# Kernel tuning notes

Hardware: AMD Instinct MI355X
Metric: run time of the kernel (lower is better)

The kernel has to match this reference:

```python
import jax, jax.numpy as jnp
import numpy as np
import math

N, E, H, NB, NL, NG, NELEM = 50000, 800000, 64, 8, 2, 64, 100
CUTOFF = 5.0


def _lin(k, fin, fout):
    kw, kb = jax.random.split(k)
    bound = 1.0 / math.sqrt(fin)
    w = jax.random.uniform(kw, (fin, fout), jnp.float32, -bound, bound)
    b = jax.random.uniform(kb, (fout,), jnp.float32, -bound, bound)
    return w, b


def setup_inputs() -> dict:
    key = jax.random.key(0)
    ks = jax.random.split(key, 12)
    z = jax.random.randint(ks[0], (N,), 0, NELEM)
    pos = jax.random.normal(ks[1], (N, 3), jnp.float32)
    edge_index = jax.random.randint(ks[2], (2, E), 0, N)
    batch = jnp.sort(jax.random.randint(ks[3], (N,), 0, NG))
    embed = jax.random.normal(ks[4], (NELEM, H), jnp.float32)
    # stacked per-interaction MLP params, leading dim = NL
    msg_w1, msg_b1, msg_w2, msg_b2 = [], [], [], []
    upd_w1, upd_b1, upd_w2, upd_b2 = [], [], [], []
    for l in range(NL):
        kl = jax.random.fold_in(ks[5], l)
        k1, k2, k3, k4 = jax.random.split(kl, 4)
        w, b = _lin(k1, 2 * H + NB, H); msg_w1.append(w); msg_b1.append(b)
        w, b = _lin(k2, H, H); msg_w2.append(w); msg_b2.append(b)
        w, b = _lin(k3, 2 * H, H); upd_w1.append(w); upd_b1.append(b)
        w, b = _lin(k4, H, H); upd_w2.append(w); upd_b2.append(b)
    eh_w1, eh_b1 = _lin(ks[6], H, H)
    eh_w2, eh_b2 = _lin(ks[7], H, 1)
    return {
        "z": z, "pos": pos, "edge_index": edge_index, "batch": batch,
        "embed": embed,
        "msg_w1": jnp.stack(msg_w1), "msg_b1": jnp.stack(msg_b1),
        "msg_w2": jnp.stack(msg_w2), "msg_b2": jnp.stack(msg_b2),
        "upd_w1": jnp.stack(upd_w1), "upd_b1": jnp.stack(upd_b1),
        "upd_w2": jnp.stack(upd_w2), "upd_b2": jnp.stack(upd_b2),
        "eh_w1": eh_w1, "eh_b1": eh_b1, "eh_w2": eh_w2, "eh_b2": eh_b2,
    }


def _mace_energy(pos, embed, msg_w1, msg_b1, msg_w2, msg_b2,
                 upd_w1, upd_b1, upd_w2, upd_b2,
                 eh_w1, eh_b1, eh_w2, eh_b2,
                 z, edge_index, batch):
    row, col = edge_index[0], edge_index[1]
    edge_vec = pos[row] - pos[col]                      # (E,3)
    d = jnp.linalg.norm(edge_vec, axis=-1)              # (E,)
    env = jnp.where(d < CUTOFF,
                    jnp.cos(d * (math.pi / (2 * CUTOFF))) ** 2,
                    0.0)
    freqs = jnp.arange(1, NB + 1, dtype=pos.dtype) * (math.pi / CUTOFF)
    d_safe = jnp.where(d > 0, d, 1.0)[:, None]
    edge_attr = jnp.sin(freqs * d[:, None]) / d_safe * env[:, None]  # (E,NB)

    x = embed[z]                                        # (N,H)
    for l in range(NL):
        # PyG source_to_target: x_j = x[row], x_i = x[col], aggregate at col
        msg_in = jnp.concatenate([x[col], x[row], edge_attr], axis=-1)  # (E,2H+NB)
        m = jax.nn.silu(msg_in @ msg_w1[l] + msg_b1[l]) @ msg_w2[l] + msg_b2[l]
        agg = jax.ops.segment_sum(m, col, num_segments=N)               # (N,H)
        u_in = jnp.concatenate([x, agg], axis=-1)
        upd = jax.nn.silu(u_in @ upd_w1[l] + upd_b1[l]) @ upd_w2[l] + upd_b2[l]
        x = x + upd

    atomic_e = jax.nn.silu(x @ eh_w1 + eh_b1) @ eh_w2 + eh_b2           # (N,1)
    energy = jax.ops.segment_sum(atomic_e, batch, num_segments=NG)      # (NG,1)
    return energy.squeeze(-1)


def reference(z, pos, edge_index, batch, embed,
              msg_w1, msg_b1, msg_w2, msg_b2,
              upd_w1, upd_b1, upd_w2, upd_b2,
              eh_w1, eh_b1, eh_w2, eh_b2):
    return _mace_energy(pos, embed, msg_w1, msg_b1, msg_w2, msg_b2,
                        upd_w1, upd_b1, upd_w2, upd_b2,
                        eh_w1, eh_b1, eh_w2, eh_b2,
                        z, edge_index, batch)
```

## Files before the change

### kernel.cpp

```cpp
#include <hip/hip_runtime.h>
#include <math.h>

#define NN 50000
#define EE 800000
#define HH 64
#define NBASIS 8
#define NLAYER 2
#define NGRAPH 64
#define NBLK1 49

using half2_t = decltype(__builtin_amdgcn_cvt_pkrtz(0.0f, 0.0f));
typedef _Float16 f16x8 __attribute__((ext_vector_type(8)));
typedef float f32x4 __attribute__((ext_vector_type(4)));

union U4H8 { uint4 u; f16x8 h; };

__device__ __forceinline__ float silu_f(float v) {
    return v * (1.0f / (1.0f + __expf(-v)));
}

__device__ __forceinline__ unsigned pk2(float a, float b) {
    union { half2_t h; unsigned u; } x;
    x.h = __builtin_amdgcn_cvt_pkrtz(a, b);
    return x.u;
}

__global__ __launch_bounds__(256) void prep_k(
    const int* __restrict__ z, const float* __restrict__ embed,
    float* __restrict__ x, unsigned* __restrict__ xh,
    const float* __restrict__ msg_w1, const float* __restrict__ msg_w2,
    const float* __restrict__ upd_w1, const float* __restrict__ upd_w2,
    const float* __restrict__ eh_w1,
    unsigned* __restrict__ w1t, unsigned* __restrict__ w2t,
    unsigned* __restrict__ w1tu, unsigned* __restrict__ w2tu,
    unsigned* __restrict__ ehw1t,
    const int* __restrict__ ecol, int* __restrict__ deg)
{
    int b = blockIdx.x;
    if (b < 6250) {
        int idx = b * 256 + threadIdx.x;
        int n = idx >> 5;
        int p = idx & 31;
        const float2* er = (const float2*)(embed + ((size_t)z[n] << 6));
        float2 v = er[p];
        ((float2*)x)[idx] = v;
        xh[idx] = pk2(v.x, v.y);
    } else if (b < 6362) {
        int idx = (b - 6250) * 256 + threadIdx.x;
        if (idx < 10240) {
            int l = idx / 5120, rem = idx % 5120;
            int f = rem / 80, kp = rem % 80;
            const float* w = msg_w1 + (size_t)l * 136 * 64;
            unsigned v = 0;
            if (kp < 68) v = pk2(w[(2*kp)*64 + f], w[(2*kp+1)*64 + f]);
            w1t[idx] = v;
        } else if (idx < 14336) {
            int j = idx - 10240;
            int l = j / 2048, rem = j % 2048;
            int n = rem / 32, kp = rem % 32;
            const float* w = msg_w2 + (size_t)l * 64 * 64;
            w2t[j] = pk2(w[(2*kp)*64 + n], w[(2*kp+1)*64 + n]);
        } else if (idx < 22528) {
            int j = idx - 14336;
            int l = j / 4096, rem = j % 4096;
            int f = rem >> 6, kp = rem & 63;
            const float* w = upd_w1 + (size_t)l * 128 * 64;
            w1tu[j] = pk2(w[(2*kp)*64 + f], w[(2*kp+1)*64 + f]);
        } else if (idx < 26624) {
            int j = idx - 22528;
            int l = j / 2048, rem = j % 2048;
            int n = rem / 32, kp = rem % 32;
            const float* w = upd_w2 + (size_t)l * 64 * 64;
            w2tu[j] = pk2(w[(2*kp)*64 + n], w[(2*kp+1)*64 + n]);
        } else if (idx < 28672) {
            int j = idx - 26624;
            int f = j / 32, kp = j % 32;
            ehw1t[j] = pk2(eh_w1[(2*kp)*64 + f], eh_w1[(2*kp+1)*64 + f]);
        }
    } else {
        int e = (b - 6362) * 256 + threadIdx.x;
        if (e < EE) atomicAdd(&deg[ecol[e]], 1);
    }
}

__global__ __launch_bounds__(1024) void scan1_k(
    const int* __restrict__ deg, int* __restrict__ cursor,
    int* __restrict__ bsum)
{
    __shared__ int wsum[16];
    int t = threadIdx.x, lane = t & 63, wave = t >> 6;
    int i = blockIdx.x * 1024 + t;
    int v = (i < NN) ? deg[i] : 0;
    int s = v;
#pragma unroll
    for (int off = 1; off < 64; off <<= 1) {
        int tv = __shfl_up(s, off, 64);
        if (lane >= off) s += tv;
    }
    if (lane == 63) wsum[wave] = s;
    __syncthreads();
    if (wave == 0) {
        int ws = (lane < 16) ? wsum[lane] : 0;
        int ss = ws;
#pragma unroll
        for (int off = 1; off < 16; off <<= 1) {
            int tv = __shfl_up(ss, off, 64);
            if (lane >= off) ss += tv;
        }
        if (lane < 16) wsum[lane] = ss - ws;
    }
    __syncthreads();
    int excl = wsum[wave] + s - v;
    if (i < NN) cursor[i] = excl;
    if (t == 1023) bsum[blockIdx.x] = excl + v;
}

__global__ __launch_bounds__(64) void scan2_k(int* __restrict__ bsum)
{
    int lane = threadIdx.x;
    int v = (lane < NBLK1) ? bsum[lane] : 0;
    int s = v;
#pragma unroll
    for (int off = 1; off < 64; off <<= 1) {
        int tv = __shfl_up(s, off, 64);
        if (lane >= off) s += tv;
    }
    if (lane < NBLK1) bsum[lane] = s - v;
}

__global__ __launch_bounds__(256) void scatter_k(
    const int* __restrict__ erow, const int* __restrict__ ecol,
    const float* __restrict__ pos,
    int* __restrict__ cursor, const int* __restrict__ bsum,
    uint4* __restrict__ edgeS)
{
    int e = blockIdx.x * 256 + threadIdx.x;
    if (e >= EE) return;
    int c = ecol[e], r = erow[e];
    int slot = atomicAdd(&cursor[c], 1) + bsum[c >> 10];
    float dx = pos[3*r]   - pos[3*c];
    float dy = pos[3*r+1] - pos[3*c+1];
    float dz = pos[3*r+2] - pos[3*c+2];
    float d = sqrtf(dx*dx + dy*dy + dz*dz);
    uint4 v;
    v.x = (unsigned)r; v.y = (unsigned)c;
    v.z = __float_as_uint(d); v.w = 0;
    edgeS[slot] = v;
}

__global__ __launch_bounds__(256, 4) void msg_k(
    const uint4* __restrict__ edgeS,
    const unsigned* __restrict__ xh,
    const unsigned* __restrict__ w1t, const float* __restrict__ b1,
    const unsigned* __restrict__ w2t, const float* __restrict__ b2,
    float* __restrict__ agg)
{
    __shared__ __align__(16) unsigned earr[4][64 * 4];
    __shared__ int ckey_s[4][64];
    __shared__ int rkey_s[4][64];
    __shared__ float Mbuf[4][64 * 33];

    const int wid  = threadIdx.x >> 6;
    const int lane = threadIdx.x & 63;
    const int q = lane >> 4, n15 = lane & 15;
    const size_t base = (size_t)blockIdx.x * 256 + wid * 64;

    int mykey;
    {
        uint4 ev = edgeS[base + lane];
        rkey_s[wid][lane] = (int)ev.x;
        mykey = (int)ev.y;
        ckey_s[wid][lane] = mykey;
        float d = __uint_as_float(ev.z);
        float env = 0.0f;
        if (d < 5.0f) {
            float cv = __cosf(d * 0.31415926535897932f);
            env = cv * cv;
        }
        float scale = (d > 0.0f) ? (env / d) : env;
        float ea[NBASIS];
#pragma unroll
        for (int k = 0; k < NBASIS; ++k)
            ea[k] = __sinf((float)(k + 1) * 0.62831853071795865f * d) * scale;
#pragma unroll
        for (int p = 0; p < 4; ++p)
            earr[wid][lane * 4 + p] = pk2(ea[2*p], ea[2*p+1]);
    }
    int pkk = __shfl_up(mykey, 1, 64);
    unsigned long long bmask = __ballot(lane > 0 && mykey != pkk);
    unsigned m32 = (unsigned)(bmask >> (lane & 32));
    __syncthreads();

    int cn[4], rn[4];
#pragma unroll
    for (int nt = 0; nt < 4; ++nt) {
        int eB = nt * 16 + n15;
        cn[nt] = ckey_s[wid][eB];
        rn[nt] = rkey_s[wid][eB];
    }

    f32x4 acc1[4][4];
#pragma unroll
    for (int mt = 0; mt < 4; ++mt) {
        f32x4 binit = *(const f32x4*)(b1 + mt * 16 + q * 4);
#pragma unroll
        for (int nt = 0; nt < 4; ++nt) acc1[mt][nt] = binit;
    }
#pragma unroll
    for (int ks = 0; ks < 5; ++ks) {
        U4H8 bfk[4];
#pragma unroll
        for (int nt = 0; nt < 4; ++nt) {
            if (ks == 4) {
                uint4 zz; zz.x = zz.y = zz.z = zz.w = 0;
                bfk[nt].u = (q == 0) ? *(const uint4*)(earr[wid] + (nt * 16 + n15) * 4) : zz;
            } else if (ks < 2) {
                bfk[nt].u = ((const uint4*)(xh + ((size_t)cn[nt] << 5)))[ks * 4 + q];
            } else {
                bfk[nt].u = ((const uint4*)(xh + ((size_t)rn[nt] << 5)))[(ks - 2) * 4 + q];
            }
        }
#pragma unroll
        for (int mt = 0; mt < 4; ++mt) {
            U4H8 af;
            af.u = *(const uint4*)(w1t + (size_t)(mt * 16 + n15) * 80 + ks * 16 + q * 4);
#pragma unroll
            for (int nt = 0; nt < 4; ++nt)
                acc1[mt][nt] = __builtin_amdgcn_mfma_f32_16x16x32_f16(
                    af.h, bfk[nt].h, acc1[mt][nt], 0, 0, 0);
        }
    }

    unsigned psrc[4][4][2];
#pragma unroll
    for (int mt = 0; mt < 4; ++mt)
#pragma unroll
        for (int nt = 0; nt < 4; ++nt) {
            psrc[mt][nt][0] = pk2(silu_f(acc1[mt][nt][0]), silu_f(acc1[mt][nt][1]));
            psrc[mt][nt][1] = pk2(silu_f(acc1[mt][nt][2]), silu_f(acc1[mt][nt][3]));
        }

    f32x4 acc2[4][4];
#pragma unroll
    for (int nt = 0; nt < 4; ++nt) {
        float b2v = b2[nt * 16 + n15];
        f32x4 binit; binit[0] = b2v; binit[1] = b2v; binit[2] = b2v; binit[3] = b2v;
#pragma unroll
        for (int et = 0; et < 4; ++et) acc2[et][nt] = binit;
    }
#pragma unroll
    for (int ks2 = 0; ks2 < 2; ++ks2) {
        U4H8 wb[4];
#pragma unroll
        for (int nt = 0; nt < 4; ++nt)
            wb[nt].u = *(const uint4*)(w2t + (size_t)(nt * 16 + n15) * 32 + ks2 * 16 + q * 4);
#pragma unroll
        for (int et = 0; et < 4; ++et) {
            unsigned tmp[4];
#pragma unroll
            for (int jr = 0; jr < 4; ++jr) {
                int srcl = (2 * (q & 1) + (jr >> 1)) * 16 + n15;
                unsigned v0 = (unsigned)__shfl((int)psrc[2 * ks2][et][jr & 1], srcl, 64);
                unsigned v1 = (unsigned)__shfl((int)psrc[2 * ks2 + 1][et][jr & 1], srcl, 64);
                tmp[jr] = (q >> 1) ? v1 : v0;
            }
            U4H8 pf;
            pf.u.x = tmp[0]; pf.u.y = tmp[1]; pf.u.z = tmp[2]; pf.u.w = tmp[3];
#pragma unroll
            for (int nt = 0; nt < 4; ++nt)
                acc2[et][nt] = __builtin_amdgcn_mfma_f32_16x16x32_f16(
                    pf.h, wb[nt].h, acc2[et][nt], 0, 0, 0);
        }
    }

#pragma unroll
    for (int hf = 0; hf < 2; ++hf) {
#pragma unroll
        for (int et = 0; et < 4; ++et)
#pragma unroll
            for (int t2 = 0; t2 < 2; ++t2) {
                int nt = 2 * hf + t2;
                int cl = t2 * 16 + n15;
                int eb = et * 16 + q * 4;
#pragma unroll
                for (int r = 0; r < 4; ++r)
                    Mbuf[wid][(eb + r) * 33 + cl] = acc2[et][nt][r];
            }
        __syncthreads();
        {
            int cl = lane & 31, st = lane >> 5;
            int ebase = 32 * st;
            float run = Mbuf[wid][ebase * 33 + cl];
            int runkey = ckey_s[wid][ebase];
            bool atstart = true;
#pragma unroll
            for (int i = 1; i < 32; ++i) {
                float v = Mbuf[wid][(ebase + i) * 33 + cl];
                if ((m32 >> i) & 1u) {
                    float* dst = agg + ((size_t)runkey << 6) + hf * 32 + cl;
                    if (atstart) atomicAdd(dst, run); else *dst = run;
                    runkey = ckey_s[wid][ebase + i]; atstart = false;
                    run = v;
                } else {
                    run += v;
                }
            }
            atomicAdd(agg + ((size_t)runkey << 6) + hf * 32 + cl, run);
        }
        __syncthreads();
    }
}

__global__ __launch_bounds__(64) void upd_k(
    float* __restrict__ x, unsigned* __restrict__ xh,
    float* __restrict__ agg,
    const unsigned* __restrict__ w1t, const float* __restrict__ b1,
    const unsigned* __restrict__ w2t, const float* __restrict__ b2,
    const unsigned* __restrict__ ehw1t, const float* __restrict__ ehb1,
    const float* __restrict__ ehw2, const float* __restrict__ ehb2,
    const int* __restrict__ batch, float* __restrict__ energy,
    int do_zero, int do_head)
{
    __shared__ float Mbuf[64 * 33];
    __shared__ float esum[NGRAPH];

    const int lane = threadIdx.x;
    const int q = lane >> 4, n15 = lane & 15;
    const int nbase = blockIdx.x * 64;

    int nc[4];
#pragma unroll
    for (int nt = 0; nt < 4; ++nt) {
        int node = nbase + nt * 16 + n15;
        nc[nt] = (node < NN) ? node : (NN - 1);
    }

    f32x4 acc1[4][4];
#pragma unroll
    for (int mt = 0; mt < 4; ++mt) {
        f32x4 binit = *(const f32x4*)(b1 + mt * 16 + q * 4);
#pragma unroll
        for (int nt = 0; nt < 4; ++nt) acc1[mt][nt] = binit;
    }
#pragma unroll
    for (int ks = 0; ks < 4; ++ks) {
        U4H8 bfk[4];
#pragma unroll
        for (int nt = 0; nt < 4; ++nt) {
            if (ks < 2) {
                bfk[nt].u = ((const uint4*)(xh + ((size_t)nc[nt] << 5)))[ks * 4 + q];
            } else {
                const float4* ap = (const float4*)(agg + ((size_t)nc[nt] << 6));
                int o = (ks - 2) * 8 + 2 * q;
                float4 a0 = ap[o], a1 = ap[o + 1];
                bfk[nt].u.x = pk2(a0.x, a0.y); bfk[nt].u.y = pk2(a0.z, a0.w);
                bfk[nt].u.z = pk2(a1.x, a1.y); bfk[nt].u.w = pk2(a1.z, a1.w);
            }
        }
#pragma unroll
        for (int mt = 0; mt < 4; ++mt) {
            U4H8 af;
            af.u = *(const uint4*)(w1t + (size_t)(mt * 16 + n15) * 64 + ks * 16 + q * 4);
#pragma unroll
            for (int nt = 0; nt < 4; ++nt)
                acc1[mt][nt] = __builtin_amdgcn_mfma_f32_16x16x32_f16(
                    af.h, bfk[nt].h, acc1[mt][nt], 0, 0, 0);
        }
    }

    unsigned psrc[4][4][2];
#pragma unroll
    for (int mt = 0; mt < 4; ++mt)
#pragma unroll
        for (int nt = 0; nt < 4; ++nt) {
            psrc[mt][nt][0] = pk2(silu_f(acc1[mt][nt][0]), silu_f(acc1[mt][nt][1]));
            psrc[mt][nt][1] = pk2(silu_f(acc1[mt][nt][2]), silu_f(acc1[mt][nt][3]));
        }

    f32x4 acc2[4][4];
#pragma unroll
    for (int nt = 0; nt < 4; ++nt) {
        float b2v = b2[nt * 16 + n15];
        f32x4 binit; binit[0] = b2v; binit[1] = b2v; binit[2] = b2v; binit[3] = b2v;
#pragma unroll
        for (int et = 0; et < 4; ++et) acc2[et][nt] = binit;
    }
#pragma unroll
    for (int ks2 = 0; ks2 < 2; ++ks2) {
        U4H8 wb[4];
#pragma unroll
        for (int nt = 0; nt < 4; ++nt)
            wb[nt].u = *(const uint4*)(w2t + (size_t)(nt * 16 + n15) * 32 + ks2 * 16 + q * 4);
#pragma unroll
        for (int et = 0; et < 4; ++et) {
            unsigned tmp[4];
#pragma unroll
            for (int jr = 0; jr < 4; ++jr) {
                int srcl = (2 * (q & 1) + (jr >> 1)) * 16 + n15;
                unsigned v0 = (unsigned)__shfl((int)psrc[2 * ks2][et][jr & 1], srcl, 64);
                unsigned v1 = (unsigned)__shfl((int)psrc[2 * ks2 + 1][et][jr & 1], srcl, 64);
                tmp[jr] = (q >> 1) ? v1 : v0;
            }
            U4H8 pf;
            pf.u.x = tmp[0]; pf.u.y = tmp[1]; pf.u.z = tmp[2]; pf.u.w = tmp[3];
#pragma unroll
            for (int nt = 0; nt < 4; ++nt)
                acc2[et][nt] = __builtin_amdgcn_mfma_f32_16x16x32_f16(
                    pf.h, wb[nt].h, acc2[et][nt], 0, 0, 0);
        }
    }

    unsigned prr[32];
#pragma unroll
    for (int p = 0; p < 32; ++p) prr[p] = 0;
#pragma unroll
    for (int hf = 0; hf < 2; ++hf) {
#pragma unroll
        for (int et = 0; et < 4; ++et)
#pragma unroll
            for (int t2 = 0; t2 < 2; ++t2) {
                int nt = 2 * hf + t2;
                int cl = t2 * 16 + n15;
                int eb = et * 16 + q * 4;
#pragma unroll
                for (int r = 0; r < 4; ++r)
                    Mbuf[(eb + r) * 33 + cl] = acc2[et][nt][r];
            }
        __syncthreads();
        {
            int node = nbase + lane;
            if (node < NN) {
                float* xr = x + ((size_t)node << 6) + hf * 32;
                unsigned* xhp = xh + ((size_t)node << 5) + hf * 16;
#pragma unroll
                for (int p = 0; p < 16; ++p) {
                    float v0 = xr[2*p]     + Mbuf[lane * 33 + 2*p];
                    float v1 = xr[2*p + 1] + Mbuf[lane * 33 + 2*p + 1];
                    xr[2*p] = v0; xr[2*p + 1] = v1;
                    unsigned pv = pk2(v0, v1);
                    xhp[p] = pv;
                    prr[hf * 16 + p] = pv;
                }
            }
        }
        __syncthreads();
    }

    if (do_zero) {
        int node = nbase + lane;
        if (node < NN) {
            float4 z4; z4.x = z4.y = z4.z = z4.w = 0.0f;
            float4* ap = (float4*)(agg + ((size_t)node << 6));
#pragma unroll
            for (int p = 0; p < 16; ++p) ap[p] = z4;
        }
    }

    if (do_head) {
        unsigned* MU = (unsigned*)Mbuf;
        esum[lane] = 0.0f;
#pragma unroll
        for (int p = 0; p < 32; ++p) MU[lane * 33 + p] = prr[p];
        __syncthreads();

        f32x4 acch[4][4];
#pragma unroll
        for (int mt = 0; mt < 4; ++mt) {
            f32x4 binit = *(const f32x4*)(ehb1 + mt * 16 + q * 4);
#pragma unroll
            for (int nt = 0; nt < 4; ++nt) acch[mt][nt] = binit;
        }
#pragma unroll
        for (int ks = 0; ks < 2; ++ks) {
            U4H8 bfk[4];
#pragma unroll
            for (int nt = 0; nt < 4; ++nt) {
                int nd = nt * 16 + n15;
                bfk[nt].u.x = MU[nd * 33 + ks * 16 + 4 * q + 0];
                bfk[nt].u.y = MU[nd * 33 + ks * 16 + 4 * q + 1];
                bfk[nt].u.z = MU[nd * 33 + ks * 16 + 4 * q + 2];
                bfk[nt].u.w = MU[nd * 33 + ks * 16 + 4 * q + 3];
            }
#pragma unroll
            for (int mt = 0; mt < 4; ++mt) {
                U4H8 af;
                af.u = *(const uint4*)(ehw1t + (size_t)(mt * 16 + n15) * 32 + ks * 16 + q * 4);
#pragma unroll
                for (int nt = 0; nt < 4; ++nt)
                    acch[mt][nt] = __builtin_amdgcn_mfma_f32_16x16x32_f16(
                        af.h, bfk[nt].h, acch[mt][nt], 0, 0, 0);
            }
        }

        f32x4 wv[4];
#pragma unroll
        for (int mt = 0; mt < 4; ++mt) wv[mt] = *(const f32x4*)(ehw2 + mt * 16 + q * 4);
        float b2v = ehb2[0];
#pragma unroll
        for (int nt = 0; nt < 4; ++nt) {
            float e = 0.0f;
#pragma unroll
            for (int mt = 0; mt < 4; ++mt)
#pragma unroll
                for (int r = 0; r < 4; ++r)
                    e = fmaf(silu_f(acch[mt][nt][r]), wv[mt][r], e);
            e += __shfl_xor(e, 16, 64);
            e += __shfl_xor(e, 32, 64);
            if (q == 0) {
                int node = nbase + nt * 16 + n15;
                if (node < NN) atomicAdd(&esum[batch[node]], e + b2v);
            }
        }
        __syncthreads();
        float v = esum[lane];
        if (v != 0.0f) atomicAdd(energy + lane, v);
    }
}

extern "C" void kernel_launch(void* const* d_in, const int* in_sizes, int n_in,
                              void* d_out, int out_size, void* d_ws, size_t ws_size,
                              hipStream_t stream) {
    const int*   z       = (const int*)  d_in[0];
    const float* pos     = (const float*)d_in[1];
    const int*   eidx    = (const int*)  d_in[2];
    const int*   batch   = (const int*)  d_in[3];
    const float* embed   = (const float*)d_in[4];
    const float* msg_w1  = (const float*)d_in[5];
    const float* msg_b1  = (const float*)d_in[6];
    const float* msg_w2  = (const float*)d_in[7];
    const float* msg_b2  = (const float*)d_in[8];
    const float* upd_w1  = (const float*)d_in[9];
    const float* upd_b1  = (const float*)d_in[10];
    const float* upd_w2  = (const float*)d_in[11];
    const float* upd_b2  = (const float*)d_in[12];
    const float* eh_w1   = (const float*)d_in[13];
    const float* eh_b1   = (const float*)d_in[14];
    const float* eh_w2   = (const float*)d_in[15];
    const float* eh_b2   = (const float*)d_in[16];

    const int* erow = eidx;
    const int* ecol = eidx + EE;

    float*    x      = (float*)d_ws;
    float*    agg    = x + (size_t)NN * HH;
    unsigned* xh     = (unsigned*)(agg + (size_t)NN * HH);
    int*      deg    = (int*)(xh + (size_t)NN * 32);
    int*      cursor = deg + NN;
    int*      bsum   = cursor + NN;
    uint4*    edgeS  = (uint4*)(bsum + 64);
    unsigned* w1t    = (unsigned*)(edgeS + EE);
    unsigned* w2t    = w1t + NLAYER * 64 * 80;
    unsigned* w1tu   = w2t + NLAYER * 64 * 32;
    unsigned* w2tu   = w1tu + NLAYER * 64 * 64;
    unsigned* ehw1t  = w2tu + NLAYER * 64 * 32;
    float*    energy = (float*)d_out;

    (void)hipMemsetAsync(energy, 0, NGRAPH * sizeof(float), stream);
    (void)hipMemsetAsync(deg, 0, NN * sizeof(int), stream);
    (void)hipMemsetAsync(agg, 0, (size_t)NN * HH * sizeof(float), stream);

    prep_k<<<9487, 256, 0, stream>>>(
        z, embed, x, xh,
        msg_w1, msg_w2, upd_w1, upd_w2, eh_w1,
        w1t, w2t, w1tu, w2tu, ehw1t,
        ecol, deg);

    scan1_k<<<NBLK1, 1024, 0, stream>>>(deg, cursor, bsum);
    scan2_k<<<1, 64, 0, stream>>>(bsum);
    scatter_k<<<(EE + 255) / 256, 256, 0, stream>>>(
        erow, ecol, pos, cursor, bsum, edgeS);

    for (int l = 0; l < NLAYER; ++l) {
        msg_k<<<EE / 256, 256, 0, stream>>>(
            edgeS, xh,
            w1t + (size_t)l * 64 * 80,
            msg_b1 + (size_t)l * HH,
            w2t + (size_t)l * 64 * 32,
            msg_b2 + (size_t)l * HH,
            agg);
        upd_k<<<(NN + 63) / 64, 64, 0, stream>>>(
            x, xh, agg,
            w1tu + (size_t)l * 64 * 64,
            upd_b1 + (size_t)l * HH,
            w2tu + (size_t)l * 64 * 32,
            upd_b2 + (size_t)l * HH,
            ehw1t, eh_b1, eh_w2, eh_b2, batch, energy,
            (l == 0) ? 1 : 0,
            (l == NLAYER - 1) ? 1 : 0);
    }
}
```

Before: 388.3 us.

## Shrink msg_k shared buffer for higher occupancy; split upd_k across four waves

msg_k now reduces its edge-message tile in four 16-column passes instead of two 32-column passes. This shrinks the per-wave shared staging buffer and raises the launch-bounds occupancy hint from 4 to 6 blocks per CU. upd_k is restructured so each block of 256 threads uses four waves, each handling 16 nodes instead of one wave handling 64. That cuts per-thread accumulator registers and increases parallelism, at the cost of more shuffles and smaller MFMA batches per wave, and the segmented-reduction loop in msg_k now has more passes and syncs.

New measurement: 724.8 us. 1.87x slower.

```diff
diff --git a/kernel.cpp b/kernel.cpp
--- a/kernel.cpp
+++ b/kernel.cpp
@@ -148,7 +148,7 @@
     edgeS[slot] = v;
 }
 
-__global__ __launch_bounds__(256, 4) void msg_k(
+__global__ __launch_bounds__(256, 6) void msg_k(
     const uint4* __restrict__ edgeS,
     const unsigned* __restrict__ xh,
     const unsigned* __restrict__ w1t, const float* __restrict__ b1,
@@ -158,7 +158,7 @@
     __shared__ __align__(16) unsigned earr[4][64 * 4];
     __shared__ int ckey_s[4][64];
     __shared__ int rkey_s[4][64];
-    __shared__ float Mbuf[4][64 * 33];
+    __shared__ float Mbuf[4][64 * 17];
 
     const int wid  = threadIdx.x >> 6;
     const int lane = threadIdx.x & 63;
@@ -188,7 +188,6 @@
     }
     int pkk = __shfl_up(mykey, 1, 64);
     unsigned long long bmask = __ballot(lane > 0 && mykey != pkk);
-    unsigned m32 = (unsigned)(bmask >> (lane & 32));
     __syncthreads();
 
     int cn[4], rn[4];
@@ -274,30 +273,25 @@
     }
 
 #pragma unroll
-    for (int hf = 0; hf < 2; ++hf) {
+    for (int hf = 0; hf < 4; ++hf) {
 #pragma unroll
         for (int et = 0; et < 4; ++et)
 #pragma unroll
-            for (int t2 = 0; t2 < 2; ++t2) {
-                int nt = 2 * hf + t2;
-                int cl = t2 * 16 + n15;
-                int eb = et * 16 + q * 4;
-#pragma unroll
-                for (int r = 0; r < 4; ++r)
-                    Mbuf[wid][(eb + r) * 33 + cl] = acc2[et][nt][r];
-            }
+            for (int r = 0; r < 4; ++r)
+                Mbuf[wid][(et * 16 + q * 4 + r) * 17 + n15] = acc2[et][hf][r];
         __syncthreads();
         {
-            int cl = lane & 31, st = lane >> 5;
-            int ebase = 32 * st;
-            float run = Mbuf[wid][ebase * 33 + cl];
+            int cl = lane & 15, st = lane >> 4;
+            int ebase = 16 * st;
+            unsigned m16 = (unsigned)(bmask >> (16 * st)) & 0xffffu;
+            float run = Mbuf[wid][ebase * 17 + cl];
             int runkey = ckey_s[wid][ebase];
             bool atstart = true;
 #pragma unroll
-            for (int i = 1; i < 32; ++i) {
-                float v = Mbuf[wid][(ebase + i) * 33 + cl];
-                if ((m32 >> i) & 1u) {
-                    float* dst = agg + ((size_t)runkey << 6) + hf * 32 + cl;
+            for (int i = 1; i < 16; ++i) {
+                float v = Mbuf[wid][(ebase + i) * 17 + cl];
+                if ((m16 >> i) & 1u) {
+                    float* dst = agg + ((size_t)runkey << 6) + hf * 16 + cl;
                     if (atstart) atomicAdd(dst, run); else *dst = run;
                     runkey = ckey_s[wid][ebase + i]; atstart = false;
                     run = v;
@@ -305,13 +299,13 @@
                     run += v;
                 }
             }
-            atomicAdd(agg + ((size_t)runkey << 6) + hf * 32 + cl, run);
+            atomicAdd(agg + ((size_t)runkey << 6) + hf * 16 + cl, run);
         }
         __syncthreads();
     }
 }
 
-__global__ __launch_bounds__(64) void upd_k(
+__global__ __launch_bounds__(256) void upd_k(
     float* __restrict__ x, unsigned* __restrict__ xh,
     float* __restrict__ agg,
     const unsigned* __restrict__ w1t, const float* __restrict__ b1,
@@ -321,199 +315,154 @@
     const int* __restrict__ batch, float* __restrict__ energy,
     int do_zero, int do_head)
 {
-    __shared__ float Mbuf[64 * 33];
+    __shared__ unsigned MU[4][16 * 33];
     __shared__ float esum[NGRAPH];
 
-    const int lane = threadIdx.x;
+    const int tid = threadIdx.x;
+    const int wid = tid >> 6;
+    const int lane = tid & 63;
     const int q = lane >> 4, n15 = lane & 15;
-    const int nbase = blockIdx.x * 64;
-
-    int nc[4];
-#pragma unroll
-    for (int nt = 0; nt < 4; ++nt) {
-        int node = nbase + nt * 16 + n15;
-        nc[nt] = (node < NN) ? node : (NN - 1);
-    }
-
-    f32x4 acc1[4][4];
-#pragma unroll
-    for (int mt = 0; mt < 4; ++mt) {
-        f32x4 binit = *(const f32x4*)(b1 + mt * 16 + q * 4);
-#pragma unroll
-        for (int nt = 0; nt < 4; ++nt) acc1[mt][nt] = binit;
-    }
+    const int base16 = blockIdx.x * 64 + wid * 16;
+
+    if (do_head) {
+        if (tid < NGRAPH) esum[tid] = 0.0f;
+        __syncthreads();
+    }
+
+    int nodeB = base16 + n15;
+    int ncB = (nodeB < NN) ? nodeB : (NN - 1);
+
+    f32x4 acc1[4];
+#pragma unroll
+    for (int mt = 0; mt < 4; ++mt)
+        acc1[mt] = *(const f32x4*)(b1 + mt * 16 + q * 4);
 #pragma unroll
     for (int ks = 0; ks < 4; ++ks) {
-        U4H8 bfk[4];
-#pragma unroll
-        for (int nt = 0; nt < 4; ++nt) {
-            if (ks < 2) {
-                bfk[nt].u = ((const uint4*)(xh + ((size_t)nc[nt] << 5)))[ks * 4 + q];
-            } else {
-                const float4* ap = (const float4*)(agg + ((size_t)nc[nt] << 6));
-                int o = (ks - 2) * 8 + 2 * q;
-                float4 a0 = ap[o], a1 = ap[o + 1];
-                bfk[nt].u.x = pk2(a0.x, a0.y); bfk[nt].u.y = pk2(a0.z, a0.w);
-                bfk[nt].u.z = pk2(a1.x, a1.y); bfk[nt].u.w = pk2(a1.z, a1.w);
-            }
+        U4H8 bfk;
+        if (ks < 2) {
+            bfk.u = ((const uint4*)(xh + ((size_t)ncB << 5)))[ks * 4 + q];
+        } else {
+            const float4* ap = (const float4*)(agg + ((size_t)ncB << 6));
+            int o = (ks - 2) * 8 + 2 * q;
+            float4 a0 = ap[o], a1 = ap[o + 1];
+            bfk.u.x = pk2(a0.x, a0.y); bfk.u.y = pk2(a0.z, a0.w);
+            bfk.u.z = pk2(a1.x, a1.y); bfk.u.w = pk2(a1.z, a1.w);
         }
 #pragma unroll
         for (int mt = 0; mt < 4; ++mt) {
             U4H8 af;
             af.u = *(const uint4*)(w1t + (size_t)(mt * 16 + n15) * 64 + ks * 16 + q * 4);
-#pragma unroll
-            for (int nt = 0; nt < 4; ++nt)
-                acc1[mt][nt] = __builtin_amdgcn_mfma_f32_16x16x32_f16(
-                    af.h, bfk[nt].h, acc1[mt][nt], 0, 0, 0);
-        }
-    }
-
-    unsigned psrc[4][4][2];
-#pragma unroll
-    for (int mt = 0; mt < 4; ++mt)
-#pragma unroll
-        for (int nt = 0; nt < 4; ++nt) {
-            psrc[mt][nt][0] = pk2(silu_f(acc1[mt][nt][0]), silu_f(acc1[mt][nt][1]));
-            psrc[mt][nt][1] = pk2(silu_f(acc1[mt][nt][2]), silu_f(acc1[mt][nt][3]));
-        }
-
-    f32x4 acc2[4][4];
+            acc1[mt] = __builtin_amdgcn_mfma_f32_16x16x32_f16(
+                af.h, bfk.h, acc1[mt], 0, 0, 0);
+        }
+    }
+
+    unsigned psrc[4][2];
+#pragma unroll
+    for (int mt = 0; mt < 4; ++mt) {
+        psrc[mt][0] = pk2(silu_f(acc1[mt][0]), silu_f(acc1[mt][1]));
+        psrc[mt][1] = pk2(silu_f(acc1[mt][2]), silu_f(acc1[mt][3]));
+    }
+
+    f32x4 acc2[4];
 #pragma unroll
     for (int nt = 0; nt < 4; ++nt) {
         float b2v = b2[nt * 16 + n15];
-        f32x4 binit; binit[0] = b2v; binit[1] = b2v; binit[2] = b2v; binit[3] = b2v;
-#pragma unroll
-        for (int et = 0; et < 4; ++et) acc2[et][nt] = binit;
+        acc2[nt][0] = b2v; acc2[nt][1] = b2v; acc2[nt][2] = b2v; acc2[nt][3] = b2v;
     }
 #pragma unroll
     for (int ks2 = 0; ks2 < 2; ++ks2) {
-        U4H8 wb[4];
-#pragma unroll
-        for (int nt = 0; nt < 4; ++nt)
-            wb[nt].u = *(const uint4*)(w2t + (size_t)(nt * 16 + n15) * 32 + ks2 * 16 + q * 4);
-#pragma unroll
-        for (int et = 0; et < 4; ++et) {
-            unsigned tmp[4];
-#pragma unroll
-            for (int jr = 0; jr < 4; ++jr) {
-                int srcl = (2 * (q & 1) + (jr >> 1)) * 16 + n15;
-                unsigned v0 = (unsigned)__shfl((int)psrc[2 * ks2][et][jr & 1], srcl, 64);
-                unsigned v1 = (unsigned)__shfl((int)psrc[2 * ks2 + 1][et][jr & 1], srcl, 64);
-                tmp[jr] = (q >> 1) ? v1 : v0;
+        unsigned tmp[4];
+#pragma unroll
+        for (int jr = 0; jr < 4; ++jr) {
+            int srcl = (2 * (q & 1) + (jr >> 1)) * 16 + n15;
+            unsigned v0 = (unsigned)__shfl((int)psrc[2 * ks2][jr & 1], srcl, 64);
+            unsigned v1 = (unsigned)__shfl((int)psrc[2 * ks2 + 1][jr & 1], srcl, 64);
+            tmp[jr] = (q >> 1) ? v1 : v0;
+        }
+        U4H8 pf;
+        pf.u.x = tmp[0]; pf.u.y = tmp[1]; pf.u.z = tmp[2]; pf.u.w = tmp[3];
+#pragma unroll
+        for (int nt = 0; nt < 4; ++nt) {
+            U4H8 wb;
+            wb.u = *(const uint4*)(w2t + (size_t)(nt * 16 + n15) * 32 + ks2 * 16 + q * 4);
+            acc2[nt] = __builtin_amdgcn_mfma_f32_16x16x32_f16(
+                pf.h, wb.h, acc2[nt], 0, 0, 0);
+        }
+    }
+
+#pragma unroll
+    for (int nt = 0; nt < 4; ++nt) {
+#pragma unroll
+        for (int r = 0; r < 4; ++r) {
+            int node = base16 + 4 * q + r;
+            float vnew = 0.0f;
+            if (node < NN) {
+                float* xp = x + ((size_t)node << 6) + nt * 16 + n15;
+                vnew = *xp + acc2[nt][r];
+                *xp = vnew;
             }
-            U4H8 pf;
-            pf.u.x = tmp[0]; pf.u.y = tmp[1]; pf.u.z = tmp[2]; pf.u.w = tmp[3];
-#pragma unroll
-            for (int nt = 0; nt < 4; ++nt)
-                acc2[et][nt] = __builtin_amdgcn_mfma_f32_16x16x32_f16(
-                    pf.h, wb[nt].h, acc2[et][nt], 0, 0, 0);
-        }
-    }
-
-    unsigned prr[32];
-#pragma unroll
-    for (int p = 0; p < 32; ++p) prr[p] = 0;
-#pragma unroll
-    for (int hf = 0; hf < 2; ++hf) {
-#pragma unroll
-        for (int et = 0; et < 4; ++et)
-#pragma unroll
-            for (int t2 = 0; t2 < 2; ++t2) {
-                int nt = 2 * hf + t2;
-                int cl = t2 * 16 + n15;
-                int eb = et * 16 + q * 4;
-#pragma unroll
-                for (int r = 0; r < 4; ++r)
-                    Mbuf[(eb + r) * 33 + cl] = acc2[et][nt][r];
+            float vpart = __shfl_xor(vnew, 1, 64);
+            if ((n15 & 1) == 0) {
+                unsigned pv = pk2(vnew, vpart);
+                int pidx = nt * 8 + (n15 >> 1);
+                MU[wid][(4 * q + r) * 33 + pidx] = pv;
+                if (node < NN) xh[((size_t)node << 5) + pidx] = pv;
             }
+        }
+    }
+
+    if (do_zero) {
+        if (nodeB < NN) {
+            float4 z4; z4.x = z4.y = z4.z = z4.w = 0.0f;
+            float4* ap = (float4*)(agg + ((size_t)nodeB << 6));
+            ap[2*q] = z4; ap[2*q + 1] = z4;
+            ap[8 + 2*q] = z4; ap[8 + 2*q + 1] = z4;
+        }
+    }
+
+    if (do_head) {
         __syncthreads();
-        {
-            int node = nbase + lane;
-            if (node < NN) {
-                float* xr = x + ((size_t)node << 6) + hf * 32;
-                unsigned* xhp = xh + ((size_t)node << 5) + hf * 16;
-#pragma unroll
-                for (int p = 0; p < 16; ++p) {
-                    float v0 = xr[2*p]     + Mbuf[lane * 33 + 2*p];
-                    float v1 = xr[2*p + 1] + Mbuf[lane * 33 + 2*p + 1];
-                    xr[2*p] = v0; xr[2*p + 1] = v1;
-                    unsigned pv = pk2(v0, v1);
-                    xhp[p] = pv;
-                    prr[hf * 16 + p] = pv;
-                }
-            }
-        }
-        __syncthreads();
-    }
-
-    if (do_zero) {
-        int node = nbase + lane;
-        if (node < NN) {
-            float4 z4; z4.x = z4.y = z4.z = z4.w = 0.0f;
-            float4* ap = (float4*)(agg + ((size_t)node << 6));
-#pragma unroll
-            for (int p = 0; p < 16; ++p) ap[p] = z4;
-        }
-    }
-
-    if (do_head) {
-        unsigned* MU = (unsigned*)Mbuf;
-        esum[lane] = 0.0f;
-#pragma unroll
-        for (int p = 0; p < 32; ++p) MU[lane * 33 + p] = prr[p];
-        __syncthreads();
-
-        f32x4 acch[4][4];
-#pragma unroll
-        for (int mt = 0; mt < 4; ++mt) {
-            f32x4 binit = *(const f32x4*)(ehb1 + mt * 16 + q * 4);
-#pragma unroll
-            for (int nt = 0; nt < 4; ++nt) acch[mt][nt] = binit;
-        }
+        f32x4 acch[4];
+#pragma unroll
+        for (int mt = 0; mt < 4; ++mt)
+            acch[mt] = *(const f32x4*)(ehb1 + mt * 16 + q * 4);
 #pragma unroll
         for (int ks = 0; ks < 2; ++ks) {
-            U4H8 bfk[4];
-#pragma unroll
-            for (int nt = 0; nt < 4; ++nt) {
-                int nd = nt * 16 + n15;
-                bfk[nt].u.x = MU[nd * 33 + ks * 16 + 4 * q + 0];
-                bfk[nt].u.y = MU[nd * 33 + ks * 16 + 4 * q + 1];
-                bfk[nt].u.z = MU[nd * 33 + ks * 16 + 4 * q + 2];
-                bfk[nt].u.w = MU[nd * 33 + ks * 16 + 4 * q + 3];
-            }
+            U4H8 bfk;
+            bfk.u.x = MU[wid][n15 * 33 + ks * 16 + 4 * q + 0];
+            bfk.u.y = MU[wid][n15 * 33 + ks * 16 + 4 * q + 1];
+            bfk.u.z = MU[wid][n15 * 33 + ks * 16 + 4 * q + 2];
+            bfk.u.w = MU[wid][n15 * 33 + ks * 16 + 4 * q + 3];
 #pragma unroll
             for (int mt = 0; mt < 4; ++mt) {
                 U4H8 af;
                 af.u = *(const uint4*)(ehw1t + (size_t)(mt * 16 + n15) * 32 + ks * 16 + q * 4);
-#pragma unroll
-                for (int nt = 0; nt < 4; ++nt)
-                    acch[mt][nt] = __builtin_amdgcn_mfma_f32_16x16x32_f16(
-                        af.h, bfk[nt].h, acch[mt][nt], 0, 0, 0);
+                acch[mt] = __builtin_amdgcn_mfma_f32_16x16x32_f16(
+                    af.h, bfk.h, acch[mt], 0, 0, 0);
             }
         }
-
         f32x4 wv[4];
 #pragma unroll
-        for (int mt = 0; mt < 4; ++mt) wv[mt] = *(const f32x4*)(ehw2 + mt * 16 + q * 4);
-        float b2v = ehb2[0];
-#pragma unroll
-        for (int nt = 0; nt < 4; ++nt) {
-            float e = 0.0f;
-#pragma unroll
-            for (int mt = 0; mt < 4; ++mt)
-#pragma unroll
-                for (int r = 0; r < 4; ++r)
-                    e = fmaf(silu_f(acch[mt][nt][r]), wv[mt][r], e);
-            e += __shfl_xor(e, 16, 64);
-            e += __shfl_xor(e, 32, 64);
-            if (q == 0) {
-                int node = nbase + nt * 16 + n15;
-                if (node < NN) atomicAdd(&esum[batch[node]], e + b2v);
-            }
+        for (int mt = 0; mt < 4; ++mt)
+            wv[mt] = *(const f32x4*)(ehw2 + mt * 16 + q * 4);
+        float e = 0.0f;
+#pragma unroll
+        for (int mt = 0; mt < 4; ++mt)
+#pragma unroll
+            for (int r = 0; r < 4; ++r)
+                e = fmaf(silu_f(acch[mt][r]), wv[mt][r], e);
+        e += __shfl_xor(e, 16, 64);
+        e += __shfl_xor(e, 32, 64);
+        if (q == 0) {
+            int node = base16 + n15;
+            if (node < NN) atomicAdd(&esum[batch[node]], e + ehb2[0]);
         }
         __syncthreads();
-        float v = esum[lane];
-        if (v != 0.0f) atomicAdd(energy + lane, v);
+        if (tid < NGRAPH) {
+            float v = esum[tid];
+            if (v != 0.0f) atomicAdd(energy + tid, v);
+        }
     }
 }
 
@@ -578,7 +527,7 @@
             w2t + (size_t)l * 64 * 32,
             msg_b2 + (size_t)l * HH,
             agg);
-        upd_k<<<(NN + 63) / 64, 64, 0, stream>>>(
+        upd_k<<<(NN + 63) / 64, 256, 0, stream>>>(
             x, xh, agg,
             w1tu + (size_t)l * 64 * 64,
             upd_b1 + (size_t)l * HH,
```
